# Optimization experiments

Measured on AMD Instinct MI355X. Metric: run time of the kernel, lower is better.

The kernel has to match this reference:

```python
import jax, jax.numpy as jnp
import numpy as np

N = 50000
E = 800000
H = 128
K_CONVS = 3
K_HOPS = 3


def setup_inputs() -> dict:
    key = jax.random.key(0)
    ks = jax.random.split(key, 8)
    x = jax.random.normal(ks[0], (N, H), dtype=jnp.float32)
    edge_index = jax.random.randint(ks[1], (2, E), 0, N, dtype=jnp.int64)
    s = 1.0 / np.sqrt(H)
    # MPlayer edge MLP: Linear(2H->H), LeakyReLU(0.2), Linear(H->H)
    W1 = jax.random.normal(ks[2], (2 * H, H), dtype=jnp.float32) * (1.0 / np.sqrt(2 * H))
    b1 = jnp.zeros((H,), jnp.float32)
    W2 = jax.random.normal(ks[3], (H, H), dtype=jnp.float32) * s
    b2 = jnp.zeros((H,), jnp.float32)
    # TAGConv stack: K_CONVS layers, each with K_HOPS+1 weight mats [H,H] + bias
    tag_w = jax.random.normal(ks[4], (K_CONVS, K_HOPS + 1, H, H), dtype=jnp.float32) * s
    tag_b = jnp.zeros((K_CONVS, H), jnp.float32)
    return {"x": x, "edge_index": edge_index, "W1": W1, "b1": b1,
            "W2": W2, "b2": b2, "tag_w": tag_w, "tag_b": tag_b}


def _mp_layer(x, src, dst, W1, b1, W2, b2):
    # gather -> concat -> 2-layer MLP per edge -> scatter-add at dst
    h = jnp.concatenate([x[dst], x[src]], axis=-1)  # [E, 2H] (x_i=dst, x_j=src)
    h = jax.nn.leaky_relu(h @ W1 + b1, negative_slope=0.2)
    m = h @ W2 + b2
    return jax.ops.segment_sum(m, dst, num_segments=N)


def _tag_conv(x, src, dst, norm, Ws, b):
    # out = sum_k A_norm^k x @ W_k + b  (PyG TAGConv, add_self_loops=False)
    out = x @ Ws[0]
    for k in range(1, Ws.shape[0]):
        x = jax.ops.segment_sum(norm[:, None] * x[src], dst, num_segments=N)
        out = out + x @ Ws[k]
    return out + b


def reference(x, edge_index, W1, b1, W2, b2, tag_w, tag_b):
    src = edge_index[0]
    dst = edge_index[1]
    # symmetric gcn_norm without self-loops (degree counted at target=dst)
    deg = jax.ops.segment_sum(jnp.ones((E,), x.dtype), dst, num_segments=N)
    dinv = jnp.where(deg > 0, jax.lax.rsqrt(jnp.maximum(deg, 1e-12)), 0.0)
    norm = dinv[src] * dinv[dst]  # [E]

    x = _mp_layer(x, src, dst, W1, b1, W2, b2)
    for i in range(K_CONVS):
        x = _tag_conv(x, src, dst, norm, tag_w[i], tag_b[i])
        x = jax.nn.relu(x)
    return x
```

## Files before the change

### kernel.cpp

```cpp
#include <hip/hip_runtime.h>

#define NN 50000
#define NE 800000
#define HH 128
#define SCAN_BLK 256
#define NBLK ((NN + SCAN_BLK - 1) / SCAN_BLK)
#define NB8 ((NN + 7) / 8)

typedef _Float16 half8 __attribute__((ext_vector_type(8)));
typedef _Float16 half4 __attribute__((ext_vector_type(4)));
typedef float floatx16 __attribute__((ext_vector_type(16)));

static inline size_t align256(size_t x) { return (x + 255) & ~(size_t)255; }

__global__ void k_deg(const int* __restrict__ dst, int* __restrict__ deg) {
    int e = blockIdx.x * 256 + threadIdx.x;
    if (e < NE) atomicAdd(&deg[dst[e]], 1);
}

__global__ void k_bsum(const int* __restrict__ deg, int* __restrict__ part) {
    __shared__ int sd[SCAN_BLK];
    int t = threadIdx.x;
    int i = blockIdx.x * SCAN_BLK + t;
    sd[t] = (i < NN) ? deg[i] : 0;
    __syncthreads();
    for (int off = SCAN_BLK / 2; off > 0; off >>= 1) {
        if (t < off) sd[t] += sd[t + off];
        __syncthreads();
    }
    if (t == 0) part[blockIdx.x] = sd[0];
}

__global__ void k_scanpart(const int* __restrict__ part, int* __restrict__ partoff) {
    __shared__ int sd[SCAN_BLK];
    int t = threadIdx.x;
    int v = (t < NBLK) ? part[t] : 0;
    sd[t] = v;
    __syncthreads();
    for (int off = 1; off < SCAN_BLK; off <<= 1) {
        int add = (t >= off) ? sd[t - off] : 0;
        __syncthreads();
        sd[t] += add;
        __syncthreads();
    }
    if (t < NBLK) partoff[t] = sd[t] - v;
}

__global__ void k_apply(const int* __restrict__ deg, const int* __restrict__ partoff,
                        int* __restrict__ offsets, float* __restrict__ dinv) {
    __shared__ int sd[SCAN_BLK];
    int t = threadIdx.x;
    int i = blockIdx.x * SCAN_BLK + t;
    int v = (i < NN) ? deg[i] : 0;
    sd[t] = v;
    __syncthreads();
    for (int off = 1; off < SCAN_BLK; off <<= 1) {
        int add = (t >= off) ? sd[t - off] : 0;
        __syncthreads();
        sd[t] += add;
        __syncthreads();
    }
    if (i < NN) {
        offsets[i] = partoff[blockIdx.x] + sd[t] - v;
        dinv[i] = (v > 0) ? rsqrtf((float)v) : 0.0f;
    }
    if (i == 0) offsets[NN] = NE;
}

__global__ void k_fill(const int* __restrict__ src, const int* __restrict__ dst,
                       const int* __restrict__ offsets, int* __restrict__ cursor,
                       int* __restrict__ csrc) {
    int e = blockIdx.x * 256 + threadIdx.x;
    if (e >= NE) return;
    int s = src[e], d = dst[e];
    int pos = atomicAdd(&cursor[d], 1);
    csrc[offsets[d] + pos] = s;
}

__global__ void k_cvt_x(const float* __restrict__ x, _Float16* __restrict__ xh) {
    int i = blockIdx.x * 256 + threadIdx.x;
    if (i * 4 < NN * HH) {
        float4 v = *(const float4*)(x + (size_t)i * 4);
        half4 h;
        h.x = (_Float16)v.x; h.y = (_Float16)v.y;
        h.z = (_Float16)v.z; h.w = (_Float16)v.w;
        *(half4*)(xh + (size_t)i * 4) = h;
    }
}

__global__ void k_cvt_w(const float* __restrict__ W1, const float* __restrict__ W2,
                        const float* __restrict__ tw,
                        _Float16* __restrict__ W1tP, _Float16* __restrict__ W1tQ,
                        _Float16* __restrict__ W2t, _Float16* __restrict__ TWt) {
    int i = blockIdx.x * 256 + threadIdx.x;
    if (i < 16384) {
        int c = i >> 7, k = i & 127;
        W1tP[c * 128 + k] = (_Float16)W1[k * 128 + c];
        W1tQ[c * 128 + k] = (_Float16)W1[(128 + k) * 128 + c];
    } else if (i < 32768) {
        int j = i - 16384;
        int c = j >> 7, k = j & 127;
        W2t[c * 128 + k] = (_Float16)W2[k * 128 + c];
    } else if (i < 32768 + 3 * 65536) {
        int j = i - 32768;
        int L = j >> 16;
        int c = (j >> 9) & 127;
        int k = j & 511;
        TWt[(size_t)L * 65536 + c * 512 + k] =
            (_Float16)tw[(size_t)L * 65536 + (size_t)(k >> 7) * 16384 + (size_t)(k & 127) * 128 + c];
    }
}

template <int KDIM, int HAS_BIAS, int HAS_DEG, int RELU, typename OutT>
__global__ __launch_bounds__(256) void k_mm(
    const _Float16* __restrict__ A, int lda,
    const _Float16* __restrict__ Bt,
    const float* __restrict__ bias, const int* __restrict__ deg,
    OutT* __restrict__ Out, int ldo, int nrows) {
    __shared__ _Float16 As[128 * 64];
    __shared__ _Float16 Bs[128 * 64];
    const int t = threadIdx.x;
    const int l = t & 63;
    const int w = t >> 6;
    const int wm = w >> 1, wn = w & 1;
    const int row0 = blockIdx.x * 128;

    floatx16 acc[2][2] = {};

    const int srow = t >> 3;
    const int sslot = t & 7;

    for (int c = 0; c < KDIM / 64; ++c) {
        __syncthreads();
#pragma unroll
        for (int p = 0; p < 4; ++p) {
            int r = srow + p * 32;
            int g = row0 + r;
            uint4 v = make_uint4(0, 0, 0, 0);
            if (g < nrows) v = *(const uint4*)(A + (size_t)g * lda + c * 64 + sslot * 8);
            *(uint4*)((char*)As + r * 128 + ((sslot * 16) ^ ((r & 7) << 4))) = v;
        }
#pragma unroll
        for (int p = 0; p < 4; ++p) {
            int r = srow + p * 32;
            uint4 v = *(const uint4*)(Bt + (size_t)r * KDIM + c * 64 + sslot * 8);
            *(uint4*)((char*)Bs + r * 128 + ((sslot * 16) ^ ((r & 7) << 4))) = v;
        }
        __syncthreads();
#pragma unroll
        for (int ks = 0; ks < 4; ++ks) {
            const int koff = ks * 32 + (l >> 5) * 16;
            half8 a0, a1, b0, b1;
            { int r = wm * 64 + (l & 31);      a0 = *(const half8*)((const char*)As + r * 128 + (koff ^ ((r & 7) << 4))); }
            { int r = wm * 64 + 32 + (l & 31); a1 = *(const half8*)((const char*)As + r * 128 + (koff ^ ((r & 7) << 4))); }
            { int r = wn * 64 + (l & 31);      b0 = *(const half8*)((const char*)Bs + r * 128 + (koff ^ ((r & 7) << 4))); }
            { int r = wn * 64 + 32 + (l & 31); b1 = *(const half8*)((const char*)Bs + r * 128 + (koff ^ ((r & 7) << 4))); }
            acc[0][0] = __builtin_amdgcn_mfma_f32_32x32x16_f16(a0, b0, acc[0][0], 0, 0, 0);
            acc[0][1] = __builtin_amdgcn_mfma_f32_32x32x16_f16(a0, b1, acc[0][1], 0, 0, 0);
            acc[1][0] = __builtin_amdgcn_mfma_f32_32x32x16_f16(a1, b0, acc[1][0], 0, 0, 0);
            acc[1][1] = __builtin_amdgcn_mfma_f32_32x32x16_f16(a1, b1, acc[1][1], 0, 0, 0);
        }
    }

#pragma unroll
    for (int mf = 0; mf < 2; ++mf) {
#pragma unroll
        for (int nf = 0; nf < 2; ++nf) {
            const int col = wn * 64 + nf * 32 + (l & 31);
            const float bc = HAS_BIAS ? bias[col] : 0.0f;
#pragma unroll
            for (int r = 0; r < 16; ++r) {
                int row = wm * 64 + mf * 32 + 4 * (l >> 5) + (r & 3) + 8 * (r >> 2);
                int g = row0 + row;
                if (g < nrows) {
                    float v = acc[mf][nf][r];
                    if (HAS_BIAS) v += (HAS_DEG ? (float)deg[g] : 1.0f) * bc;
                    if (RELU) v = fmaxf(v, 0.0f);
                    Out[(size_t)g * ldo + col] = (OutT)v;
                }
            }
        }
    }
}

__global__ __launch_bounds__(256) void k_edge_mp(_Float16* __restrict__ PQ,
                                                 const int* __restrict__ offsets,
                                                 const int* __restrict__ csrc) {
    const int t = threadIdx.x;
    const int n = blockIdx.x * 8 + (t >> 5);
    if (n >= NN) return;
    const int lane = t & 31;
    const int beg = offsets[n], end = offsets[n + 1];
    half4 p4 = *(const half4*)(PQ + (size_t)n * 256 + lane * 4);
    const float p0 = (float)p4.x, p1 = (float)p4.y, p2 = (float)p4.z, p3 = (float)p4.w;
    float a0 = 0.f, a1 = 0.f, a2 = 0.f, a3 = 0.f;
    int i = beg;
#define LRELU4(vx, vy, vz, vw)                                        \
    a0 += ((vx) > 0.f) ? (vx) : 0.2f * (vx);                          \
    a1 += ((vy) > 0.f) ? (vy) : 0.2f * (vy);                          \
    a2 += ((vz) > 0.f) ? (vz) : 0.2f * (vz);                          \
    a3 += ((vw) > 0.f) ? (vw) : 0.2f * (vw);
    for (; i + 4 <= end; i += 4) {
        int s0 = csrc[i + 0], s1 = csrc[i + 1], s2 = csrc[i + 2], s3 = csrc[i + 3];
        half4 q0 = *(const half4*)(PQ + (size_t)s0 * 256 + 128 + lane * 4);
        half4 q1 = *(const half4*)(PQ + (size_t)s1 * 256 + 128 + lane * 4);
        half4 q2 = *(const half4*)(PQ + (size_t)s2 * 256 + 128 + lane * 4);
        half4 q3 = *(const half4*)(PQ + (size_t)s3 * 256 + 128 + lane * 4);
        LRELU4(p0 + (float)q0.x, p1 + (float)q0.y, p2 + (float)q0.z, p3 + (float)q0.w)
        LRELU4(p0 + (float)q1.x, p1 + (float)q1.y, p2 + (float)q1.z, p3 + (float)q1.w)
        LRELU4(p0 + (float)q2.x, p1 + (float)q2.y, p2 + (float)q2.z, p3 + (float)q2.w)
        LRELU4(p0 + (float)q3.x, p1 + (float)q3.y, p2 + (float)q3.z, p3 + (float)q3.w)
    }
    for (; i < end; ++i) {
        int s = csrc[i];
        half4 q = *(const half4*)(PQ + (size_t)s * 256 + 128 + lane * 4);
        LRELU4(p0 + (float)q.x, p1 + (float)q.y, p2 + (float)q.z, p3 + (float)q.w)
    }
#undef LRELU4
    half4 o;
    o.x = (_Float16)a0; o.y = (_Float16)a1; o.z = (_Float16)a2; o.w = (_Float16)a3;
    *(half4*)(PQ + (size_t)n * 256 + lane * 4) = o;
}

__global__ __launch_bounds__(256) void k_spmm(const _Float16* __restrict__ Xin,
                                              _Float16* __restrict__ Yout,
                                              const int* __restrict__ offsets,
                                              const int* __restrict__ csrc,
                                              const float* __restrict__ dinv) {
    const int t = threadIdx.x;
    const int n = blockIdx.x * 8 + (t >> 5);
    if (n >= NN) return;
    const int lane = t & 31;
    const int beg = offsets[n], end = offsets[n + 1];
    const float dn = dinv[n];
    float a0 = 0.f, a1 = 0.f, a2 = 0.f, a3 = 0.f;
    int i = beg;
    for (; i + 4 <= end; i += 4) {
        int s0 = csrc[i + 0], s1 = csrc[i + 1], s2 = csrc[i + 2], s3 = csrc[i + 3];
        float n0 = dinv[s0], n1 = dinv[s1], n2 = dinv[s2], n3 = dinv[s3];
        half4 v0 = *(const half4*)(Xin + (size_t)s0 * 512 + lane * 4);
        half4 v1 = *(const half4*)(Xin + (size_t)s1 * 512 + lane * 4);
        half4 v2 = *(const half4*)(Xin + (size_t)s2 * 512 + lane * 4);
        half4 v3 = *(const half4*)(Xin + (size_t)s3 * 512 + lane * 4);
        a0 += n0 * (float)v0.x + n1 * (float)v1.x + n2 * (float)v2.x + n3 * (float)v3.x;
        a1 += n0 * (float)v0.y + n1 * (float)v1.y + n2 * (float)v2.y + n3 * (float)v3.y;
        a2 += n0 * (float)v0.z + n1 * (float)v1.z + n2 * (float)v2.z + n3 * (float)v3.z;
        a3 += n0 * (float)v0.w + n1 * (float)v1.w + n2 * (float)v2.w + n3 * (float)v3.w;
    }
    for (; i < end; ++i) {
        int s = csrc[i];
        float nv = dinv[s];
        half4 v = *(const half4*)(Xin + (size_t)s * 512 + lane * 4);
        a0 += nv * (float)v.x; a1 += nv * (float)v.y;
        a2 += nv * (float)v.z; a3 += nv * (float)v.w;
    }
    half4 o;
    o.x = (_Float16)(dn * a0); o.y = (_Float16)(dn * a1);
    o.z = (_Float16)(dn * a2); o.w = (_Float16)(dn * a3);
    *(half4*)(Yout + (size_t)n * 512 + lane * 4) = o;
}

extern "C" void kernel_launch(void* const* d_in, const int* in_sizes, int n_in,
                              void* d_out, int out_size, void* d_ws, size_t ws_size,
                              hipStream_t stream) {
    const float* x  = (const float*)d_in[0];
    const int*   ei = (const int*)d_in[1];
    const float* W1 = (const float*)d_in[2];
    const float* b1 = (const float*)d_in[3];
    const float* W2 = (const float*)d_in[4];
    const float* b2 = (const float*)d_in[5];
    const float* tw = (const float*)d_in[6];
    const float* tb = (const float*)d_in[7];
    float* out = (float*)d_out;

    const int* srcp = ei;
    const int* dstp = ei + NE;

    char* p = (char*)d_ws;
    auto alloc = [&](size_t bytes) { char* r = p; p += align256(bytes); return r; };
    int*       deg     = (int*)alloc((size_t)NN * 4);
    int*       cursor  = (int*)alloc((size_t)NN * 4);
    int*       offsets = (int*)alloc((size_t)(NN + 1) * 4);
    float*     dinv    = (float*)alloc((size_t)NN * 4);
    int*       part    = (int*)alloc((size_t)NBLK * 4);
    int*       partoff = (int*)alloc((size_t)NBLK * 4);
    int*       csrc    = (int*)alloc((size_t)NE * 4);
    _Float16*  xh      = (_Float16*)alloc((size_t)NN * HH * 2);
    _Float16*  PQ      = (_Float16*)alloc((size_t)NN * 256 * 2);
    _Float16*  X4      = (_Float16*)alloc((size_t)NN * 512 * 2);
    _Float16*  W1tP    = (_Float16*)alloc(16384 * 2);
    _Float16*  W1tQ    = (_Float16*)alloc(16384 * 2);
    _Float16*  W2t     = (_Float16*)alloc(16384 * 2);
    _Float16*  TWt     = (_Float16*)alloc((size_t)3 * 65536 * 2);

    hipMemsetAsync(deg, 0, (size_t)NN * 4, stream);
    hipMemsetAsync(cursor, 0, (size_t)NN * 4, stream);

    k_deg<<<(NE + 255) / 256, 256, 0, stream>>>(dstp, deg);
    k_bsum<<<NBLK, SCAN_BLK, 0, stream>>>(deg, part);
    k_scanpart<<<1, SCAN_BLK, 0, stream>>>(part, partoff);
    k_apply<<<NBLK, SCAN_BLK, 0, stream>>>(deg, partoff, offsets, dinv);
    k_fill<<<(NE + 255) / 256, 256, 0, stream>>>(srcp, dstp, offsets, cursor, csrc);

    k_cvt_x<<<(NN * HH / 4 + 255) / 256, 256, 0, stream>>>(x, xh);
    k_cvt_w<<<(32768 + 3 * 65536 + 255) / 256, 256, 0, stream>>>(W1, W2, tw, W1tP, W1tQ, W2t, TWt);

    const int mmgrid = (NN + 127) / 128;

    k_mm<128, 1, 0, 0, _Float16><<<mmgrid, 256, 0, stream>>>(xh, HH, W1tP, b1, nullptr, PQ, 256, NN);
    k_mm<128, 0, 0, 0, _Float16><<<mmgrid, 256, 0, stream>>>(xh, HH, W1tQ, nullptr, nullptr, PQ + 128, 256, NN);
    k_edge_mp<<<NB8, 256, 0, stream>>>(PQ, offsets, csrc);
    k_mm<128, 1, 1, 0, _Float16><<<mmgrid, 256, 0, stream>>>(PQ, 256, W2t, b2, deg, X4, 512, NN);

    for (int L = 0; L < 3; ++L) {
        const _Float16* Wt = TWt + (size_t)L * 65536;
        const float* bL = tb + (size_t)L * 128;
        k_spmm<<<NB8, 256, 0, stream>>>(X4 + 0,   X4 + 128, offsets, csrc, dinv);
        k_spmm<<<NB8, 256, 0, stream>>>(X4 + 128, X4 + 256, offsets, csrc, dinv);
        k_spmm<<<NB8, 256, 0, stream>>>(X4 + 256, X4 + 384, offsets, csrc, dinv);
        if (L < 2) {
            k_mm<512, 1, 0, 1, _Float16><<<mmgrid, 256, 0, stream>>>(X4, 512, Wt, bL, nullptr, X4, 512, NN);
        } else {
            k_mm<512, 1, 0, 1, float><<<mmgrid, 256, 0, stream>>>(X4, 512, Wt, bL, nullptr, out, HH, NN);
        }
    }
}
```

Before: 530.1 us.

## Partition node features into 16-column panels so gathers stay cache-resident

Stores P, Q and the four hop buffers as eight column panels of 16 halves per node (panel-major), and changes the edge and SpMM kernels so each block handles one panel for 64 nodes. Each gather then touches a 32-byte slice within a ~1.6 MB panel, meant to raise L2/MALL hit rates for the random source-row gathers. The GEMM kernel gains modes to read and write this panel layout. CSR indices are loaded nontemporally. The trade-off is that the edge list and offsets are re-read eight times and GEMM loads become strided.

Measured after the change: 1.166 ms. +119.9%, slower.

```diff
diff --git a/kernel.cpp b/kernel.cpp
--- a/kernel.cpp
+++ b/kernel.cpp
@@ -5,7 +5,8 @@
 #define HH 128
 #define SCAN_BLK 256
 #define NBLK ((NN + SCAN_BLK - 1) / SCAN_BLK)
-#define NB8 ((NN + 7) / 8)
+#define NGB ((NN + 63) / 64)
+#define PSZ ((size_t)NN * 16)
 
 typedef _Float16 half8 __attribute__((ext_vector_type(8)));
 typedef _Float16 half4 __attribute__((ext_vector_type(4)));
@@ -111,7 +112,7 @@
     }
 }
 
-template <int KDIM, int HAS_BIAS, int HAS_DEG, int RELU, typename OutT>
+template <int KDIM, int A_MODE, int HAS_BIAS, int HAS_DEG, int RELU, int OUT_MODE, typename OutT>
 __global__ __launch_bounds__(256) void k_mm(
     const _Float16* __restrict__ A, int lda,
     const _Float16* __restrict__ Bt,
@@ -133,16 +134,23 @@
     for (int c = 0; c < KDIM / 64; ++c) {
         __syncthreads();
 #pragma unroll
-        for (int p = 0; p < 4; ++p) {
-            int r = srow + p * 32;
+        for (int p4 = 0; p4 < 4; ++p4) {
+            int r = srow + p4 * 32;
             int g = row0 + r;
             uint4 v = make_uint4(0, 0, 0, 0);
-            if (g < nrows) v = *(const uint4*)(A + (size_t)g * lda + c * 64 + sslot * 8);
+            if (g < nrows) {
+                if (A_MODE == 0) {
+                    v = *(const uint4*)(A + (size_t)g * lda + c * 64 + sslot * 8);
+                } else {
+                    int k = c * 64 + sslot * 8;
+                    v = *(const uint4*)(A + ((size_t)(k >> 4) * NN + g) * 16 + (k & 15));
+                }
+            }
             *(uint4*)((char*)As + r * 128 + ((sslot * 16) ^ ((r & 7) << 4))) = v;
         }
 #pragma unroll
-        for (int p = 0; p < 4; ++p) {
-            int r = srow + p * 32;
+        for (int p4 = 0; p4 < 4; ++p4) {
+            int r = srow + p4 * 32;
             uint4 v = *(const uint4*)(Bt + (size_t)r * KDIM + c * 64 + sslot * 8);
             *(uint4*)((char*)Bs + r * 128 + ((sslot * 16) ^ ((r & 7) << 4))) = v;
         }
@@ -176,23 +184,31 @@
                     float v = acc[mf][nf][r];
                     if (HAS_BIAS) v += (HAS_DEG ? (float)deg[g] : 1.0f) * bc;
                     if (RELU) v = fmaxf(v, 0.0f);
-                    Out[(size_t)g * ldo + col] = (OutT)v;
+                    if (OUT_MODE == 0) {
+                        Out[(size_t)g * ldo + col] = (OutT)v;
+                    } else {
+                        Out[((size_t)(col >> 4) * NN + g) * 16 + (col & 15)] = (OutT)v;
+                    }
                 }
             }
         }
     }
 }
 
-__global__ __launch_bounds__(256) void k_edge_mp(_Float16* __restrict__ PQ,
+__global__ __launch_bounds__(256) void k_edge_mp(_Float16* __restrict__ P,
+                                                 const _Float16* __restrict__ Q,
                                                  const int* __restrict__ offsets,
                                                  const int* __restrict__ csrc) {
     const int t = threadIdx.x;
-    const int n = blockIdx.x * 8 + (t >> 5);
+    const int c = blockIdx.x & 7;
+    const int n = (blockIdx.x >> 3) * 64 + (t >> 2);
     if (n >= NN) return;
-    const int lane = t & 31;
+    const int off = (t & 3) * 4;
+    _Float16* prow = P + ((size_t)c * NN + n) * 16 + off;
+    const _Float16* Qb = Q + (size_t)c * NN * 16;
+    half4 pv = *(const half4*)prow;
+    const float p0 = (float)pv.x, p1 = (float)pv.y, p2 = (float)pv.z, p3 = (float)pv.w;
     const int beg = offsets[n], end = offsets[n + 1];
-    half4 p4 = *(const half4*)(PQ + (size_t)n * 256 + lane * 4);
-    const float p0 = (float)p4.x, p1 = (float)p4.y, p2 = (float)p4.z, p3 = (float)p4.w;
     float a0 = 0.f, a1 = 0.f, a2 = 0.f, a3 = 0.f;
     int i = beg;
 #define LRELU4(vx, vy, vz, vw)                                        \
@@ -201,25 +217,28 @@
     a2 += ((vz) > 0.f) ? (vz) : 0.2f * (vz);                          \
     a3 += ((vw) > 0.f) ? (vw) : 0.2f * (vw);
     for (; i + 4 <= end; i += 4) {
-        int s0 = csrc[i + 0], s1 = csrc[i + 1], s2 = csrc[i + 2], s3 = csrc[i + 3];
-        half4 q0 = *(const half4*)(PQ + (size_t)s0 * 256 + 128 + lane * 4);
-        half4 q1 = *(const half4*)(PQ + (size_t)s1 * 256 + 128 + lane * 4);
-        half4 q2 = *(const half4*)(PQ + (size_t)s2 * 256 + 128 + lane * 4);
-        half4 q3 = *(const half4*)(PQ + (size_t)s3 * 256 + 128 + lane * 4);
+        int s0 = __builtin_nontemporal_load(csrc + i + 0);
+        int s1 = __builtin_nontemporal_load(csrc + i + 1);
+        int s2 = __builtin_nontemporal_load(csrc + i + 2);
+        int s3 = __builtin_nontemporal_load(csrc + i + 3);
+        half4 q0 = *(const half4*)(Qb + (size_t)s0 * 16 + off);
+        half4 q1 = *(const half4*)(Qb + (size_t)s1 * 16 + off);
+        half4 q2 = *(const half4*)(Qb + (size_t)s2 * 16 + off);
+        half4 q3 = *(const half4*)(Qb + (size_t)s3 * 16 + off);
         LRELU4(p0 + (float)q0.x, p1 + (float)q0.y, p2 + (float)q0.z, p3 + (float)q0.w)
         LRELU4(p0 + (float)q1.x, p1 + (float)q1.y, p2 + (float)q1.z, p3 + (float)q1.w)
         LRELU4(p0 + (float)q2.x, p1 + (float)q2.y, p2 + (float)q2.z, p3 + (float)q2.w)
         LRELU4(p0 + (float)q3.x, p1 + (float)q3.y, p2 + (float)q3.z, p3 + (float)q3.w)
     }
     for (; i < end; ++i) {
-        int s = csrc[i];
-        half4 q = *(const half4*)(PQ + (size_t)s * 256 + 128 + lane * 4);
+        int s = __builtin_nontemporal_load(csrc + i);
+        half4 q = *(const half4*)(Qb + (size_t)s * 16 + off);
         LRELU4(p0 + (float)q.x, p1 + (float)q.y, p2 + (float)q.z, p3 + (float)q.w)
     }
 #undef LRELU4
     half4 o;
     o.x = (_Float16)a0; o.y = (_Float16)a1; o.z = (_Float16)a2; o.w = (_Float16)a3;
-    *(half4*)(PQ + (size_t)n * 256 + lane * 4) = o;
+    *(half4*)prow = o;
 }
 
 __global__ __launch_bounds__(256) void k_spmm(const _Float16* __restrict__ Xin,
@@ -228,36 +247,41 @@
                                               const int* __restrict__ csrc,
                                               const float* __restrict__ dinv) {
     const int t = threadIdx.x;
-    const int n = blockIdx.x * 8 + (t >> 5);
+    const int c = blockIdx.x & 7;
+    const int n = (blockIdx.x >> 3) * 64 + (t >> 2);
     if (n >= NN) return;
-    const int lane = t & 31;
+    const int off = (t & 3) * 4;
+    const _Float16* Xb = Xin + (size_t)c * NN * 16;
     const int beg = offsets[n], end = offsets[n + 1];
     const float dn = dinv[n];
     float a0 = 0.f, a1 = 0.f, a2 = 0.f, a3 = 0.f;
     int i = beg;
     for (; i + 4 <= end; i += 4) {
-        int s0 = csrc[i + 0], s1 = csrc[i + 1], s2 = csrc[i + 2], s3 = csrc[i + 3];
+        int s0 = __builtin_nontemporal_load(csrc + i + 0);
+        int s1 = __builtin_nontemporal_load(csrc + i + 1);
+        int s2 = __builtin_nontemporal_load(csrc + i + 2);
+        int s3 = __builtin_nontemporal_load(csrc + i + 3);
         float n0 = dinv[s0], n1 = dinv[s1], n2 = dinv[s2], n3 = dinv[s3];
-        half4 v0 = *(const half4*)(Xin + (size_t)s0 * 512 + lane * 4);
-        half4 v1 = *(const half4*)(Xin + (size_t)s1 * 512 + lane * 4);
-        half4 v2 = *(const half4*)(Xin + (size_t)s2 * 512 + lane * 4);
-        half4 v3 = *(const half4*)(Xin + (size_t)s3 * 512 + lane * 4);
+        half4 v0 = *(const half4*)(Xb + (size_t)s0 * 16 + off);
+        half4 v1 = *(const half4*)(Xb + (size_t)s1 * 16 + off);
+        half4 v2 = *(const half4*)(Xb + (size_t)s2 * 16 + off);
+        half4 v3 = *(const half4*)(Xb + (size_t)s3 * 16 + off);
         a0 += n0 * (float)v0.x + n1 * (float)v1.x + n2 * (float)v2.x + n3 * (float)v3.x;
         a1 += n0 * (float)v0.y + n1 * (float)v1.y + n2 * (float)v2.y + n3 * (float)v3.y;
         a2 += n0 * (float)v0.z + n1 * (float)v1.z + n2 * (float)v2.z + n3 * (float)v3.z;
         a3 += n0 * (float)v0.w + n1 * (float)v1.w + n2 * (float)v2.w + n3 * (float)v3.w;
     }
     for (; i < end; ++i) {
-        int s = csrc[i];
+        int s = __builtin_nontemporal_load(csrc + i);
         float nv = dinv[s];
-        half4 v = *(const half4*)(Xin + (size_t)s * 512 + lane * 4);
+        half4 v = *(const half4*)(Xb + (size_t)s * 16 + off);
         a0 += nv * (float)v.x; a1 += nv * (float)v.y;
         a2 += nv * (float)v.z; a3 += nv * (float)v.w;
     }
     half4 o;
     o.x = (_Float16)(dn * a0); o.y = (_Float16)(dn * a1);
     o.z = (_Float16)(dn * a2); o.w = (_Float16)(dn * a3);
-    *(half4*)(Yout + (size_t)n * 512 + lane * 4) = o;
+    *(half4*)(Yout + ((size_t)c * NN + n) * 16 + off) = o;
 }
 
 extern "C" void kernel_launch(void* const* d_in, const int* in_sizes, int n_in,
@@ -286,8 +310,9 @@
     int*       partoff = (int*)alloc((size_t)NBLK * 4);
     int*       csrc    = (int*)alloc((size_t)NE * 4);
     _Float16*  xh      = (_Float16*)alloc((size_t)NN * HH * 2);
-    _Float16*  PQ      = (_Float16*)alloc((size_t)NN * 256 * 2);
-    _Float16*  X4      = (_Float16*)alloc((size_t)NN * 512 * 2);
+    _Float16*  Pp      = (_Float16*)alloc(8 * PSZ * 2);
+    _Float16*  Qp      = (_Float16*)alloc(8 * PSZ * 2);
+    _Float16*  X4      = (_Float16*)alloc(32 * PSZ * 2);
     _Float16*  W1tP    = (_Float16*)alloc(16384 * 2);
     _Float16*  W1tQ    = (_Float16*)alloc(16384 * 2);
     _Float16*  W2t     = (_Float16*)alloc(16384 * 2);
@@ -306,22 +331,23 @@
     k_cvt_w<<<(32768 + 3 * 65536 + 255) / 256, 256, 0, stream>>>(W1, W2, tw, W1tP, W1tQ, W2t, TWt);
 
     const int mmgrid = (NN + 127) / 128;
-
-    k_mm<128, 1, 0, 0, _Float16><<<mmgrid, 256, 0, stream>>>(xh, HH, W1tP, b1, nullptr, PQ, 256, NN);
-    k_mm<128, 0, 0, 0, _Float16><<<mmgrid, 256, 0, stream>>>(xh, HH, W1tQ, nullptr, nullptr, PQ + 128, 256, NN);
-    k_edge_mp<<<NB8, 256, 0, stream>>>(PQ, offsets, csrc);
-    k_mm<128, 1, 1, 0, _Float16><<<mmgrid, 256, 0, stream>>>(PQ, 256, W2t, b2, deg, X4, 512, NN);
+    const int ggrid = 8 * NGB;
+
+    k_mm<128, 0, 1, 0, 0, 1, _Float16><<<mmgrid, 256, 0, stream>>>(xh, HH, W1tP, b1, nullptr, Pp, 0, NN);
+    k_mm<128, 0, 0, 0, 0, 1, _Float16><<<mmgrid, 256, 0, stream>>>(xh, HH, W1tQ, nullptr, nullptr, Qp, 0, NN);
+    k_edge_mp<<<ggrid, 256, 0, stream>>>(Pp, Qp, offsets, csrc);
+    k_mm<128, 1, 1, 1, 0, 1, _Float16><<<mmgrid, 256, 0, stream>>>(Pp, 0, W2t, b2, deg, X4, 0, NN);
 
     for (int L = 0; L < 3; ++L) {
         const _Float16* Wt = TWt + (size_t)L * 65536;
         const float* bL = tb + (size_t)L * 128;
-        k_spmm<<<NB8, 256, 0, stream>>>(X4 + 0,   X4 + 128, offsets, csrc, dinv);
-        k_spmm<<<NB8, 256, 0, stream>>>(X4 + 128, X4 + 256, offsets, csrc, dinv);
-        k_spmm<<<NB8, 256, 0, stream>>>(X4 + 256, X4 + 384, offsets, csrc, dinv);
+        k_spmm<<<ggrid, 256, 0, stream>>>(X4 + 0 * 8 * PSZ, X4 + 1 * 8 * PSZ, offsets, csrc, dinv);
+        k_spmm<<<ggrid, 256, 0, stream>>>(X4 + 1 * 8 * PSZ, X4 + 2 * 8 * PSZ, offsets, csrc, dinv);
+        k_spmm<<<ggrid, 256, 0, stream>>>(X4 + 2 * 8 * PSZ, X4 + 3 * 8 * PSZ, offsets, csrc, dinv);
         if (L < 2) {
-            k_mm<512, 1, 0, 1, _Float16><<<mmgrid, 256, 0, stream>>>(X4, 512, Wt, bL, nullptr, X4, 512, NN);
+            k_mm<512, 1, 1, 0, 1, 1, _Float16><<<mmgrid, 256, 0, stream>>>(X4, 0, Wt, bL, nullptr, X4, 0, NN);
         } else {
-            k_mm<512, 1, 0, 1, float><<<mmgrid, 256, 0, stream>>>(X4, 512, Wt, bL, nullptr, out, HH, NN);
-        }
-    }
-}
+            k_mm<512, 1, 1, 0, 1, 0, float><<<mmgrid, 256, 0, stream>>>(X4, 0, Wt, bL, nullptr, out, HH, NN);
+        }
+    }
+}
```
